# Kernel optimization log

Measured on AMD Instinct MI355X. Metric: run time of the kernel, lower is better.

## Reference

```python
import jax, jax.numpy as jnp
import numpy as np

SCALE = 64 ** 0.5  # hardcoded in original module regardless of dims


def setup_inputs() -> dict:
    key = jax.random.key(0)
    kx, kw = jax.random.split(key)
    B, S, D, O = 8, 2048, 512, 512
    x = jax.random.normal(kx, (B, S, D), dtype=jnp.float32)
    kernel = jax.random.normal(kw, (3, D, O), dtype=jnp.float32) * 0.02
    return {"x": x, "kernel": kernel}


def reference(x, kernel):
    # x: [B, S, D], kernel: [3, D, O]
    WQ = jnp.einsum('bsd,do->bso', x, kernel[0])
    WK = jnp.einsum('bsd,do->bso', x, kernel[1])
    WV = jnp.einsum('bsd,do->bso', x, kernel[2])
    QK = jnp.einsum('bso,bto->bst', WQ, WK)  # [B, S, S]
    # argmin of row-sums, taken from batch element 0 and applied to all batches
    # (faithful to c[0] in the original TF code)
    row_sums = jnp.sum(QK, axis=2)          # [B, S]
    c0 = jnp.argmin(row_sums[0])            # scalar index
    # Original removes row c0, scales, softmaxes remaining rows over last axis,
    # then re-inserts a zero row at c0. Softmax is row-independent, so this is
    # equivalent to softmax on all rows followed by zeroing row c0.
    A = jax.nn.softmax(QK / SCALE, axis=-1)  # [B, S, S]
    row_mask = (jnp.arange(QK.shape[1]) == c0)[None, :, None]
    A = jnp.where(row_mask, jnp.zeros((), A.dtype), A)
    V = jnp.einsum('bst,bto->bso', A, WV)    # [B, S, O]
    return V
```

## Files before the change

kernel.cpp:

```cpp
#include <hip/hip_runtime.h>
#include <stdint.h>

typedef __attribute__((ext_vector_type(8))) short short8;
typedef __attribute__((ext_vector_type(4))) float f32x4;

__device__ __forceinline__ float bf2f(unsigned short u) {
  union { unsigned int i; float f; } x; x.i = ((unsigned int)u) << 16; return x.f;
}
__device__ __forceinline__ unsigned short f2bf(float f) {
  union { float f; unsigned int i; } x; x.f = f;
  unsigned int u = x.i;
  unsigned int r = (u + 0x7FFFu + ((u >> 16) & 1u)) >> 16;
  return (unsigned short)r;
}
__device__ __forceinline__ unsigned int fmono(float f) {
  unsigned int u = __float_as_uint(f);
  return (u & 0x80000000u) ? ~u : (u | 0x80000000u);
}

typedef const __attribute__((address_space(1))) void* gas_ptr;
typedef __attribute__((address_space(3))) void* las_ptr;
__device__ __forceinline__ void gld_lds16(const void* g, void* l) {
  __builtin_amdgcn_global_load_lds((gas_ptr)g, (las_ptr)l, 16, 0, 0);
}

__global__ void cvt_kernel(const float* __restrict__ x, unsigned short* __restrict__ xbf,
                           const float* __restrict__ kern, unsigned short* __restrict__ wbfT) {
  int bid = blockIdx.x;
  if (bid < 4096) {
    int i = bid * 256 + threadIdx.x;
    const float4* xp = (const float4*)x;
    float4 a = xp[2 * i], b = xp[2 * i + 1];
    union { unsigned short us[8]; uint4 v; } o;
    o.us[0] = f2bf(a.x); o.us[1] = f2bf(a.y); o.us[2] = f2bf(a.z); o.us[3] = f2bf(a.w);
    o.us[4] = f2bf(b.x); o.us[5] = f2bf(b.y); o.us[6] = f2bf(b.z); o.us[7] = f2bf(b.w);
    ((uint4*)xbf)[i] = o.v;
  } else {
    __shared__ float tile[32][33];
    int b = bid - 4096;
    int w = b >> 8;
    int r2 = b & 255;
    int d0 = (r2 >> 4) * 32, o0 = (r2 & 15) * 32;
    int c = threadIdx.x & 31, r0 = threadIdx.x >> 5;
    const float* kp = kern + (size_t)w * 262144;
    unsigned short* op = wbfT + (size_t)w * 262144;
#pragma unroll
    for (int i = 0; i < 4; ++i)
      tile[r0 + 8 * i][c] = kp[(size_t)(d0 + r0 + 8 * i) * 512 + o0 + c];
    __syncthreads();
#pragma unroll
    for (int i = 0; i < 4; ++i)
      op[(size_t)(o0 + r0 + 8 * i) * 512 + d0 + c] = f2bf(tile[c][r0 + 8 * i]);
  }
}

template <int MODE, int BNT>
__device__ __forceinline__ void gemm_body(
    int bid, int nwg, char* lds,
    const unsigned short* __restrict__ A, const unsigned short* __restrict__ B,
    void* __restrict__ C, int M, int N, int K,
    long long Abat, long long Bbat, long long Cbat, float scale,
    const unsigned long long* __restrict__ keyp) {
  constexpr int LB = BNT / 128;
  constexpr int BHB = (BNT / 2) * 128;
  constexpr int PBUF = 32768 + 2 * BHB;
  constexpr int WM = (BNT == 128) ? 4 : 2;
  constexpr int RPW = 256 / WM;
  constexpr int MF = RPW / 16;
  constexpr int IC = MF / 4;

  const int tx = N / BNT, ty = M >> 8;
  const int swz = (bid & 7) * (nwg >> 3) + (bid >> 3);
  const int tpz = tx * ty;
  const int z = swz / tpz;
  const int rem = swz - z * tpz;
  const int by = rem / tx;
  const int bx = rem - by * tx;
  const unsigned short* Ab = A + (size_t)z * (size_t)Abat;
  const unsigned short* Bb = B + (size_t)z * (size_t)Bbat;
  const int bm0 = by << 8;
  const int bn0 = bx * BNT;

  const int tid = threadIdx.x, lane = tid & 63, w = tid >> 6;
  const int wr = (WM == 4) ? (w >> 1) : (w >> 2);
  const int wc = (WM == 4) ? (w & 1) : (w & 3);
  const int ln15 = lane & 15, hi = lane >> 4;
  const unsigned xorv = (unsigned)(lane & 7) << 4;
  const unsigned K2 = (unsigned)K * 2;

  const char* gsrc[4];
  gsrc[0] = (const char*)(Ab + (size_t)bm0 * K);
  gsrc[1] = (const char*)(Ab + (size_t)(bm0 + 128) * K);
  gsrc[2] = (const char*)(Bb + (size_t)bn0 * K);
  gsrc[3] = (const char*)(Bb + (size_t)(bn0 + BNT / 2) * K);
  const int hoff_[4] = {0, 16384, 32768, 32768 + BHB};
  unsigned op0 = (unsigned)(w * 1024 + lane * 16);
  unsigned op1 = op0 + 8192;
  const unsigned soff0 = (op0 >> 7) * K2 + ((op0 & 127) ^ (((op0 >> 7) & 7) << 4));
  const unsigned soff1 = (op1 >> 7) * K2 + ((op1 & 127) ^ (((op1 >> 7) & 7) << 4));
  const int lb0 = w * 1024, lb1 = 8192 + w * 1024;

#define STAGE(h, pp, kb)                                              \
  do {                                                                \
    char* lp_ = lds + (pp) * PBUF + hoff_[h];                         \
    const char* gp_ = gsrc[h] + ((unsigned)(kb) << 1);                \
    gld_lds16(gp_ + soff0, lp_ + lb0);                                \
    if ((h) < 2 || LB == 2) gld_lds16(gp_ + soff1, lp_ + lb1);        \
  } while (0)

  f32x4 acc[MF][4];
#pragma unroll
  for (int i = 0; i < MF; ++i)
#pragma unroll
    for (int j = 0; j < 4; ++j) acc[i][j] = (f32x4){0.f, 0.f, 0.f, 0.f};

  f32x4 accs1[MF];
  short8 onesf;
  if constexpr (MODE == 2) {
#pragma unroll
    for (int i = 0; i < MF; ++i) accs1[i] = (f32x4){0.f, 0.f, 0.f, 0.f};
#pragma unroll
    for (int j = 0; j < 8; ++j) onesf[j] = (short)0x3F80;
  }

  const int NT = K >> 6;
  STAGE(0, 0, 0);
  STAGE(1, 0, 0);
  STAGE(2, 0, 0);
  STAGE(3, 0, 0);
  asm volatile("s_waitcnt vmcnt(0)" ::: "memory");
  __builtin_amdgcn_s_barrier();

  short8 bfrag[4][2];
  for (int t = 0; t < NT; ++t) {
    const int p = t & 1;
    char* Lp = lds + p * PBUF;
    const int kN = (t + 1) << 6;
    const bool sN = (t + 1 < NT);
#pragma unroll
    for (int q = 0; q < 4; ++q) {
      if (q == 0) {
#pragma unroll
        for (int nf = 0; nf < 4; ++nf) {
          const int col = wc * 64 + nf * 16 + ln15;
          const char* bp = Lp + 32768 + ((col >= BNT / 2) ? BHB : 0) +
                           (col & (BNT / 2 - 1)) * 128;
#pragma unroll
          for (int k = 0; k < 2; ++k)
            bfrag[nf][k] = *(const short8*)(bp + (((unsigned)(k * 64 + hi * 16)) ^ xorv));
        }
      }
      short8 af[IC][2];
#pragma unroll
      for (int i = 0; i < IC; ++i) {
        const int row = wr * RPW + (q * IC + i) * 16 + ln15;
        const char* ap = Lp + ((row >> 7) << 14) + (row & 127) * 128;
#pragma unroll
        for (int k = 0; k < 2; ++k)
          af[i][k] = *(const short8*)(ap + (((unsigned)(k * 64 + hi * 16)) ^ xorv));
      }
      if (q == 0 && sN) { STAGE(0, p ^ 1, kN); STAGE(2, p ^ 1, kN); }
      if (q == 1 && sN) { STAGE(1, p ^ 1, kN); STAGE(3, p ^ 1, kN); }
      __builtin_amdgcn_s_setprio(1);
#pragma unroll
      for (int i = 0; i < IC; ++i) {
#pragma unroll
        for (int nf = 0; nf < 4; ++nf)
#pragma unroll
          for (int k = 0; k < 2; ++k)
            acc[q * IC + i][nf] = __builtin_amdgcn_mfma_f32_16x16x32_bf16(
                af[i][k], bfrag[nf][k], acc[q * IC + i][nf], 0, 0, 0);
        if constexpr (MODE == 2) {
#pragma unroll
          for (int k = 0; k < 2; ++k)
            accs1[q * IC + i] = __builtin_amdgcn_mfma_f32_16x16x32_bf16(
                af[i][k], onesf, accs1[q * IC + i], 0, 0, 0);
        }
      }
      __builtin_amdgcn_s_setprio(0);
    }
    asm volatile("s_waitcnt vmcnt(0) lgkmcnt(0)" ::: "memory");
    __builtin_amdgcn_s_barrier();
  }
#undef STAGE

  const int rg = hi * 4;
  const int cc = ln15;
  int c0 = 0;
  if constexpr (MODE == 2) c0 = (int)(unsigned int)(*keyp & 0xffffffffULL);
#pragma unroll
  for (int mf = 0; mf < MF; ++mf) {
#pragma unroll
    for (int nf = 0; nf < 4; ++nf) {
#pragma unroll
      for (int r = 0; r < 4; ++r) {
        int m = bm0 + wr * RPW + mf * 16 + rg + r;
        int n = bn0 + wc * 64 + nf * 16 + cc;
        float v = acc[mf][nf][r];
        if (MODE == 0) {
          ((unsigned short*)C)[(size_t)z * (size_t)Cbat + (size_t)m * N + n] =
              f2bf(__expf(v * scale));
        } else if (MODE == 1) {
          int bb = n >> 11, tl = n & 2047;
          ((unsigned short*)C)[((size_t)(bb * 512 + m) << 11) + tl] = f2bf(v);
        } else if (MODE == 2) {
          float lv = (m == c0) ? 0.f : (1.f / accs1[mf][r]);
          ((float*)C)[(size_t)z * (size_t)Cbat + (size_t)m * N + n] = v * lv;
        } else {
          size_t idx = (size_t)(n >> 9) * 8388608 + (size_t)m * 512 + (n & 511);
          float sc = (n >> 9) ? 1.0f : 0.125f;
          ((unsigned short*)C)[idx] = f2bf(v * sc);
        }
      }
    }
  }
}

template <int MODE, int BNT>
__global__ __launch_bounds__(512, 1) void gemm8p(
    const unsigned short* __restrict__ A, const unsigned short* __restrict__ B,
    void* __restrict__ C, int M, int N, int K,
    long long Abat, long long Bbat, long long Cbat, float scale,
    const unsigned long long* __restrict__ keyp) {
  constexpr int PBUF = 32768 + 2 * ((BNT / 2) * 128);
  __shared__ __align__(16) char lds[2 * PBUF];
  gemm_body<MODE, BNT>(blockIdx.x, gridDim.x, lds, A, B, C, M, N, K,
                       Abat, Bbat, Cbat, scale, keyp);
}

__global__ __launch_bounds__(512, 1) void proj_fused(
    const unsigned short* __restrict__ xbf, const unsigned short* __restrict__ wbfT,
    unsigned short* __restrict__ WQ, unsigned short* __restrict__ VT) {
  __shared__ __align__(16) char lds[131072];
  int bid = blockIdx.x;
  if (bid < 256) {
    gemm_body<3, 256>(bid, 256, lds, xbf, wbfT, WQ, 16384, 1024, 512,
                      0, 0, 0, 1.0f, nullptr);
  } else {
    gemm_body<1, 128>(bid - 256, 256, lds, wbfT + 524288, xbf, VT, 512, 16384, 512,
                      0, 0, 0, 1.0f, nullptr);
  }
}

__global__ void ksum_kernel(const unsigned short* __restrict__ WK, float* __restrict__ partial) {
  int col = threadIdx.x;
  int t0 = blockIdx.x * 64;
  float s = 0.f;
  for (int t = 0; t < 64; ++t) s += bf2f(WK[(size_t)(t0 + t) * 512 + col]);
  partial[blockIdx.x * 512 + col] = s;
}

__global__ void rs_argmin_kernel(const unsigned short* __restrict__ WQ,
                                 const float* __restrict__ partial,
                                 unsigned long long* __restrict__ key) {
  __shared__ __align__(16) float ks[512];
  int tid = threadIdx.x;
  for (int c = tid; c < 512; c += 256) {
    float s = 0.f;
#pragma unroll
    for (int j = 0; j < 32; ++j) s += partial[j * 512 + c];
    ks[c] = s;
  }
  __syncthreads();
  int w = tid >> 6, lane = tid & 63;
  float4 ka = *(const float4*)&ks[lane * 8];
  float4 kb = *(const float4*)&ks[lane * 8 + 4];
  for (int it = 0; it < 16; ++it) {
    int row = blockIdx.x * 64 + w * 16 + it;
    uint4 q = *(const uint4*)(WQ + (size_t)row * 512 + lane * 8);
    float d = 0.f;
    d += bf2f((unsigned short)(q.x & 0xffff)) * ka.x;
    d += bf2f((unsigned short)(q.x >> 16)) * ka.y;
    d += bf2f((unsigned short)(q.y & 0xffff)) * ka.z;
    d += bf2f((unsigned short)(q.y >> 16)) * ka.w;
    d += bf2f((unsigned short)(q.z & 0xffff)) * kb.x;
    d += bf2f((unsigned short)(q.z >> 16)) * kb.y;
    d += bf2f((unsigned short)(q.w & 0xffff)) * kb.z;
    d += bf2f((unsigned short)(q.w >> 16)) * kb.w;
#pragma unroll
    for (int m = 32; m; m >>= 1) d += __shfl_xor(d, m);
    if (lane == 0) {
      unsigned long long kk = ((unsigned long long)fmono(d) << 32) | (unsigned int)row;
      atomicMin(key, kk);
    }
  }
}

extern "C" void kernel_launch(void* const* d_in, const int* in_sizes, int n_in,
                              void* d_out, int out_size, void* d_ws, size_t ws_size,
                              hipStream_t stream) {
  const float* x = (const float*)d_in[0];
  const float* kern = (const float*)d_in[1];
  float* out = (float*)d_out;

  char* ws = (char*)d_ws;
  size_t off = 0;
  auto alloc = [&](size_t b) -> char* {
    char* p = ws + off;
    off += (b + 255) & ~(size_t)255;
    return p;
  };
  unsigned short* xbf = (unsigned short*)alloc(16384ull * 512 * 2);
  unsigned short* wbfT = (unsigned short*)alloc(3ull * 512 * 512 * 2);
  unsigned short* WQ = (unsigned short*)alloc(16384ull * 512 * 2);
  unsigned short* WK = (unsigned short*)alloc(16384ull * 512 * 2);
  unsigned short* VT = (unsigned short*)alloc(16384ull * 512 * 2);
  float* partial = (float*)alloc(32ull * 512 * 4);
  unsigned long long* key = (unsigned long long*)alloc(256);
  size_t fixed = off;
  size_t sbytes = 2048ull * 2048 * 2;
  int nb = 1;
  if (ws_size > fixed + sbytes) {
    size_t av = (ws_size - fixed) / sbytes;
    nb = av > 8 ? 8 : (int)av;
    if (nb < 1) nb = 1;
  }
  unsigned short* S = (unsigned short*)alloc(sbytes * (size_t)nb);

  hipMemsetAsync(key, 0xFF, 8, stream);

  cvt_kernel<<<4864, 256, 0, stream>>>(x, xbf, kern, wbfT);

  proj_fused<<<512, 512, 0, stream>>>(xbf, wbfT, WQ, VT);

  ksum_kernel<<<32, 512, 0, stream>>>(WK, partial);
  rs_argmin_kernel<<<32, 256, 0, stream>>>(WQ, partial, key);

  for (int b0 = 0; b0 < 8; b0 += nb) {
    int cb = (8 - b0) < nb ? (8 - b0) : nb;
    gemm8p<0, 256><<<64 * cb, 512, 0, stream>>>(
        WQ + (size_t)b0 * 2048 * 512, WK + (size_t)b0 * 2048 * 512, S,
        2048, 2048, 512, 2048ll * 512, 2048ll * 512, 2048ll * 2048, 1.0f,
        nullptr);
    gemm8p<2, 128><<<32 * cb, 512, 0, stream>>>(
        S, VT + (size_t)b0 * 512 * 2048, out + (size_t)b0 * 2048 * 512,
        2048, 512, 2048, 2048ll * 2048, 512ll * 2048, 2048ll * 512, 1.0f,
        key);
  }
}
```

Baseline: 162.2 us.

## Split K across wave pairs in PV GEMM with LDS reduction

Replaces the generic MODE 2 path of the shared GEMM body with a dedicated P·V kernel. In it, wave pairs split each 64-wide K step, each wave taking half the K slice, instead of every wave computing its full row set over all of K. Partial accumulators and row-sum accumulators are exchanged through LDS, summed, and each wave then writes half of the output rows with normalization and row-c0 zeroing. The goal is fewer serial MFMA and LDS fragment reads per wave and a smaller per-wave accumulator footprint. The cost is an extra LDS reduction phase with barriers at the end.

```diff
diff --git a/kernel.cpp b/kernel.cpp
--- a/kernel.cpp
+++ b/kernel.cpp
@@ -114,15 +114,6 @@
 #pragma unroll
     for (int j = 0; j < 4; ++j) acc[i][j] = (f32x4){0.f, 0.f, 0.f, 0.f};
 
-  f32x4 accs1[MF];
-  short8 onesf;
-  if constexpr (MODE == 2) {
-#pragma unroll
-    for (int i = 0; i < MF; ++i) accs1[i] = (f32x4){0.f, 0.f, 0.f, 0.f};
-#pragma unroll
-    for (int j = 0; j < 8; ++j) onesf[j] = (short)0x3F80;
-  }
-
   const int NT = K >> 6;
   STAGE(0, 0, 0);
   STAGE(1, 0, 0);
@@ -170,12 +161,6 @@
           for (int k = 0; k < 2; ++k)
             acc[q * IC + i][nf] = __builtin_amdgcn_mfma_f32_16x16x32_bf16(
                 af[i][k], bfrag[nf][k], acc[q * IC + i][nf], 0, 0, 0);
-        if constexpr (MODE == 2) {
-#pragma unroll
-          for (int k = 0; k < 2; ++k)
-            accs1[q * IC + i] = __builtin_amdgcn_mfma_f32_16x16x32_bf16(
-                af[i][k], onesf, accs1[q * IC + i], 0, 0, 0);
-        }
       }
       __builtin_amdgcn_s_setprio(0);
     }
@@ -186,8 +171,6 @@
 
   const int rg = hi * 4;
   const int cc = ln15;
-  int c0 = 0;
-  if constexpr (MODE == 2) c0 = (int)(unsigned int)(*keyp & 0xffffffffULL);
 #pragma unroll
   for (int mf = 0; mf < MF; ++mf) {
 #pragma unroll
@@ -203,9 +186,6 @@
         } else if (MODE == 1) {
           int bb = n >> 11, tl = n & 2047;
           ((unsigned short*)C)[((size_t)(bb * 512 + m) << 11) + tl] = f2bf(v);
-        } else if (MODE == 2) {
-          float lv = (m == c0) ? 0.f : (1.f / accs1[mf][r]);
-          ((float*)C)[(size_t)z * (size_t)Cbat + (size_t)m * N + n] = v * lv;
         } else {
           size_t idx = (size_t)(n >> 9) * 8388608 + (size_t)m * 512 + (n & 511);
           float sc = (n >> 9) ? 1.0f : 0.125f;
@@ -239,6 +219,165 @@
   } else {
     gemm_body<1, 128>(bid - 256, 256, lds, wbfT + 524288, xbf, VT, 512, 16384, 512,
                       0, 0, 0, 1.0f, nullptr);
+  }
+}
+
+__global__ __launch_bounds__(512, 1) void gemm_pv(
+    const unsigned short* __restrict__ A, const unsigned short* __restrict__ B,
+    float* __restrict__ C, int N, long long Abat, long long Bbat, long long Cbat,
+    const unsigned long long* __restrict__ keyp) {
+  constexpr int PBUF = 49152;
+  __shared__ __align__(16) char lds[2 * PBUF];
+  const int K = 2048;
+  const int tx = N >> 7;
+  const int nwg = gridDim.x;
+  const int bid = blockIdx.x;
+  const int swz = (bid & 7) * (nwg >> 3) + (bid >> 3);
+  const int tpz = tx * 8;
+  const int z = swz / tpz;
+  const int rem = swz - z * tpz;
+  const int by = rem / tx;
+  const int bx = rem - by * tx;
+  const unsigned short* Ab = A + (size_t)z * (size_t)Abat;
+  const unsigned short* Bb = B + (size_t)z * (size_t)Bbat;
+  const int bm0 = by << 8;
+  const int bn0 = bx << 7;
+
+  const int tid = threadIdx.x, lane = tid & 63, w = tid >> 6;
+  const int wk = w & 1, wc = (w >> 1) & 1, wr = w >> 2;
+  const int ln15 = lane & 15, hi = lane >> 4;
+  const unsigned xorv = (unsigned)(lane & 7) << 4;
+  const unsigned K2 = (unsigned)K * 2;
+
+  const char* gsrc[4];
+  gsrc[0] = (const char*)(Ab + (size_t)bm0 * K);
+  gsrc[1] = (const char*)(Ab + (size_t)(bm0 + 128) * K);
+  gsrc[2] = (const char*)(Bb + (size_t)bn0 * K);
+  gsrc[3] = (const char*)(Bb + (size_t)(bn0 + 64) * K);
+  const int hoff_[4] = {0, 16384, 32768, 40960};
+  unsigned op0 = (unsigned)(w * 1024 + lane * 16);
+  unsigned op1 = op0 + 8192;
+  const unsigned soff0 = (op0 >> 7) * K2 + ((op0 & 127) ^ (((op0 >> 7) & 7) << 4));
+  const unsigned soff1 = (op1 >> 7) * K2 + ((op1 & 127) ^ (((op1 >> 7) & 7) << 4));
+  const int lb0 = w * 1024, lb1 = 8192 + w * 1024;
+
+#define STAGE(h, pp, kb)                                              \
+  do {                                                                \
+    char* lp_ = lds + (pp) * PBUF + hoff_[h];                         \
+    const char* gp_ = gsrc[h] + ((unsigned)(kb) << 1);                \
+    gld_lds16(gp_ + soff0, lp_ + lb0);                                \
+    if ((h) < 2) gld_lds16(gp_ + soff1, lp_ + lb1);                   \
+  } while (0)
+
+  f32x4 acc[8][4];
+  f32x4 accs1[8];
+#pragma unroll
+  for (int i = 0; i < 8; ++i) {
+#pragma unroll
+    for (int j = 0; j < 4; ++j) acc[i][j] = (f32x4){0.f, 0.f, 0.f, 0.f};
+    accs1[i] = (f32x4){0.f, 0.f, 0.f, 0.f};
+  }
+  short8 onesf;
+#pragma unroll
+  for (int j = 0; j < 8; ++j) onesf[j] = (short)0x3F80;
+
+  const unsigned koff = ((unsigned)(wk * 64 + hi * 16)) ^ xorv;
+
+  const int NT = 32;
+  STAGE(0, 0, 0);
+  STAGE(1, 0, 0);
+  STAGE(2, 0, 0);
+  STAGE(3, 0, 0);
+  asm volatile("s_waitcnt vmcnt(0)" ::: "memory");
+  __builtin_amdgcn_s_barrier();
+
+  short8 bfrag[4];
+  for (int t = 0; t < NT; ++t) {
+    const int p = t & 1;
+    char* Lp = lds + p * PBUF;
+    const int kN = (t + 1) << 6;
+    const bool sN = (t + 1 < NT);
+#pragma unroll
+    for (int q = 0; q < 4; ++q) {
+      if (q == 0) {
+#pragma unroll
+        for (int nf = 0; nf < 4; ++nf) {
+          const int col = wc * 64 + nf * 16 + ln15;
+          const char* bp = Lp + 32768 + ((col >= 64) ? 8192 : 0) + (col & 63) * 128;
+          bfrag[nf] = *(const short8*)(bp + koff);
+        }
+      }
+      short8 af[2];
+#pragma unroll
+      for (int i = 0; i < 2; ++i) {
+        const int row = wr * 128 + (q * 2 + i) * 16 + ln15;
+        const char* ap = Lp + ((row >> 7) << 14) + (row & 127) * 128;
+        af[i] = *(const short8*)(ap + koff);
+      }
+      if (q == 0 && sN) { STAGE(0, p ^ 1, kN); STAGE(2, p ^ 1, kN); }
+      if (q == 1 && sN) { STAGE(1, p ^ 1, kN); STAGE(3, p ^ 1, kN); }
+      __builtin_amdgcn_s_setprio(1);
+#pragma unroll
+      for (int i = 0; i < 2; ++i) {
+#pragma unroll
+        for (int nf = 0; nf < 4; ++nf)
+          acc[q * 2 + i][nf] = __builtin_amdgcn_mfma_f32_16x16x32_bf16(
+              af[i], bfrag[nf], acc[q * 2 + i][nf], 0, 0, 0);
+        accs1[q * 2 + i] = __builtin_amdgcn_mfma_f32_16x16x32_bf16(
+            af[i], onesf, accs1[q * 2 + i], 0, 0, 0);
+      }
+      __builtin_amdgcn_s_setprio(0);
+    }
+    asm volatile("s_waitcnt vmcnt(0) lgkmcnt(0)" ::: "memory");
+    __builtin_amdgcn_s_barrier();
+  }
+#undef STAGE
+
+  const int give0 = wk ? 0 : 4;
+  const int recv0 = wk ? 4 : 0;
+  char* wp = lds + w * 12288 + lane * 192;
+  const char* rp = lds + (w ^ 1) * 12288 + lane * 192;
+#pragma unroll
+  for (int r2 = 0; r2 < 2; ++r2) {
+#pragma unroll
+    for (int m2 = 0; m2 < 2; ++m2) {
+#pragma unroll
+      for (int nf = 0; nf < 4; ++nf)
+        *(f32x4*)(wp + (m2 * 4 + nf) * 16) = acc[give0 + r2 * 2 + m2][nf];
+      *(f32x4*)(wp + (8 + m2) * 16) = accs1[give0 + r2 * 2 + m2];
+    }
+    asm volatile("s_waitcnt lgkmcnt(0)" ::: "memory");
+    __builtin_amdgcn_s_barrier();
+#pragma unroll
+    for (int m2 = 0; m2 < 2; ++m2) {
+#pragma unroll
+      for (int nf = 0; nf < 4; ++nf) {
+        f32x4 pv = *(const f32x4*)(rp + (m2 * 4 + nf) * 16);
+        acc[recv0 + r2 * 2 + m2][nf] += pv;
+      }
+      f32x4 ps = *(const f32x4*)(rp + (8 + m2) * 16);
+      accs1[recv0 + r2 * 2 + m2] += ps;
+    }
+    asm volatile("s_waitcnt lgkmcnt(0)" ::: "memory");
+    __builtin_amdgcn_s_barrier();
+  }
+
+  const int rg = hi * 4;
+  const int cc = ln15;
+  const int c0 = (int)(unsigned int)(*keyp & 0xffffffffULL);
+#pragma unroll
+  for (int kf = 0; kf < 4; ++kf) {
+    const int mf = recv0 + kf;
+#pragma unroll
+    for (int nf = 0; nf < 4; ++nf) {
+#pragma unroll
+      for (int r = 0; r < 4; ++r) {
+        int m = bm0 + wr * 128 + mf * 16 + rg + r;
+        int n = bn0 + wc * 64 + nf * 16 + cc;
+        float lv = (m == c0) ? 0.f : (1.f / accs1[mf][r]);
+        C[(size_t)z * (size_t)Cbat + (size_t)m * N + n] = acc[mf][nf][r] * lv;
+      }
+    }
   }
 }
 
@@ -332,9 +471,9 @@
         WQ + (size_t)b0 * 2048 * 512, WK + (size_t)b0 * 2048 * 512, S,
         2048, 2048, 512, 2048ll * 512, 2048ll * 512, 2048ll * 2048, 1.0f,
         nullptr);
-    gemm8p<2, 128><<<32 * cb, 512, 0, stream>>>(
+    gemm_pv<<<32 * cb, 512, 0, stream>>>(
         S, VT + (size_t)b0 * 512 * 2048, out + (size_t)b0 * 2048 * 512,
-        2048, 512, 2048, 2048ll * 2048, 512ll * 2048, 2048ll * 512, 1.0f,
+        512, 2048ll * 2048, 512ll * 2048, 2048ll * 512,
         key);
   }
 }
```

New measurement: 226.9 us. 39.8% more time.

## Store exp scores and V in fp8 and run PV GEMM with fp8 MFMA

Applied to the files above, without the earlier changes.

The exponentiated score matrix is now written as fp8 (e4m3) instead of bf16, halving its memory traffic. V is stored as a two-term fp8 split (high part plus residual), and a new dedicated fp8 PV GEMM kernel uses the fp8 MFMA instruction with row sums computed via a ones vector. This cuts S write/read bandwidth and uses faster fp8 matrix instructions, at the cost of reduced precision for the softmax probabilities and extra MFMAs for the V residual.

```diff
diff --git a/kernel.cpp b/kernel.cpp
--- a/kernel.cpp
+++ b/kernel.cpp
@@ -3,6 +3,7 @@
 
 typedef __attribute__((ext_vector_type(8))) short short8;
 typedef __attribute__((ext_vector_type(4))) float f32x4;
+typedef long long i64;
 
 __device__ __forceinline__ float bf2f(unsigned short u) {
   union { unsigned int i; float f; } x; x.i = ((unsigned int)u) << 16; return x.f;
@@ -16,6 +17,28 @@
 __device__ __forceinline__ unsigned int fmono(float f) {
   unsigned int u = __float_as_uint(f);
   return (u & 0x80000000u) ? ~u : (u | 0x80000000u);
+}
+
+__device__ __forceinline__ unsigned char f2fp8(float f) {
+  unsigned int u = __float_as_uint(f);
+  unsigned int s = (u >> 24) & 0x80u;
+  unsigned int av = u & 0x7fffffffu;
+  if (av >= 0x43E00000u) return (unsigned char)(s | 0x7E);
+  if (av < 0x3C800000u) {
+    int mi = (int)rintf(fabsf(__uint_as_float(av)) * 512.f);
+    return (unsigned char)(s | (unsigned)mi);
+  }
+  unsigned int r = av + 0x7FFFFu + ((av >> 20) & 1u);
+  unsigned int e = (r >> 23) - 120u;
+  unsigned int m3 = (r >> 20) & 7u;
+  if (e > 15u) return (unsigned char)(s | 0x7E);
+  return (unsigned char)(s | (e << 3) | m3);
+}
+__device__ __forceinline__ float fp8dec(unsigned char b) {
+  int s = b >> 7, e = (b >> 3) & 15, m = b & 7;
+  float v = e ? __uint_as_float(((unsigned)(e + 120) << 23) | ((unsigned)m << 20))
+              : (float)m * 0.001953125f;
+  return s ? -v : v;
 }
 
 typedef const __attribute__((address_space(1))) void* gas_ptr;
@@ -59,8 +82,7 @@
     int bid, int nwg, char* lds,
     const unsigned short* __restrict__ A, const unsigned short* __restrict__ B,
     void* __restrict__ C, int M, int N, int K,
-    long long Abat, long long Bbat, long long Cbat, float scale,
-    const unsigned long long* __restrict__ keyp) {
+    long long Abat, long long Bbat, long long Cbat, float scale) {
   constexpr int LB = BNT / 128;
   constexpr int BHB = (BNT / 2) * 128;
   constexpr int PBUF = 32768 + 2 * BHB;
@@ -114,15 +136,6 @@
 #pragma unroll
     for (int j = 0; j < 4; ++j) acc[i][j] = (f32x4){0.f, 0.f, 0.f, 0.f};
 
-  f32x4 accs1[MF];
-  short8 onesf;
-  if constexpr (MODE == 2) {
-#pragma unroll
-    for (int i = 0; i < MF; ++i) accs1[i] = (f32x4){0.f, 0.f, 0.f, 0.f};
-#pragma unroll
-    for (int j = 0; j < 8; ++j) onesf[j] = (short)0x3F80;
-  }
-
   const int NT = K >> 6;
   STAGE(0, 0, 0);
   STAGE(1, 0, 0);
@@ -170,12 +183,6 @@
           for (int k = 0; k < 2; ++k)
             acc[q * IC + i][nf] = __builtin_amdgcn_mfma_f32_16x16x32_bf16(
                 af[i][k], bfrag[nf][k], acc[q * IC + i][nf], 0, 0, 0);
-        if constexpr (MODE == 2) {
-#pragma unroll
-          for (int k = 0; k < 2; ++k)
-            accs1[q * IC + i] = __builtin_amdgcn_mfma_f32_16x16x32_bf16(
-                af[i][k], onesf, accs1[q * IC + i], 0, 0, 0);
-        }
       }
       __builtin_amdgcn_s_setprio(0);
     }
@@ -186,8 +193,6 @@
 
   const int rg = hi * 4;
   const int cc = ln15;
-  int c0 = 0;
-  if constexpr (MODE == 2) c0 = (int)(unsigned int)(*keyp & 0xffffffffULL);
 #pragma unroll
   for (int mf = 0; mf < MF; ++mf) {
 #pragma unroll
@@ -198,14 +203,14 @@
         int n = bn0 + wc * 64 + nf * 16 + cc;
         float v = acc[mf][nf][r];
         if (MODE == 0) {
-          ((unsigned short*)C)[(size_t)z * (size_t)Cbat + (size_t)m * N + n] =
-              f2bf(__expf(v * scale));
+          ((unsigned char*)C)[(size_t)z * (size_t)Cbat + (size_t)m * N + n] =
+              f2fp8(__expf(v * scale));
         } else if (MODE == 1) {
           int bb = n >> 11, tl = n & 2047;
-          ((unsigned short*)C)[((size_t)(bb * 512 + m) << 11) + tl] = f2bf(v);
-        } else if (MODE == 2) {
-          float lv = (m == c0) ? 0.f : (1.f / accs1[mf][r]);
-          ((float*)C)[(size_t)z * (size_t)Cbat + (size_t)m * N + n] = v * lv;
+          size_t idx = ((size_t)(bb * 512 + m) << 11) + tl;
+          unsigned char bhi = f2fp8(v);
+          ((unsigned char*)C)[idx] = bhi;
+          ((unsigned char*)C)[idx + 8388608] = f2fp8(v - fp8dec(bhi));
         } else {
           size_t idx = (size_t)(n >> 9) * 8388608 + (size_t)m * 512 + (n & 511);
           float sc = (n >> 9) ? 1.0f : 0.125f;
@@ -220,25 +225,153 @@
 __global__ __launch_bounds__(512, 1) void gemm8p(
     const unsigned short* __restrict__ A, const unsigned short* __restrict__ B,
     void* __restrict__ C, int M, int N, int K,
-    long long Abat, long long Bbat, long long Cbat, float scale,
-    const unsigned long long* __restrict__ keyp) {
+    long long Abat, long long Bbat, long long Cbat, float scale) {
   constexpr int PBUF = 32768 + 2 * ((BNT / 2) * 128);
   __shared__ __align__(16) char lds[2 * PBUF];
   gemm_body<MODE, BNT>(blockIdx.x, gridDim.x, lds, A, B, C, M, N, K,
-                       Abat, Bbat, Cbat, scale, keyp);
+                       Abat, Bbat, Cbat, scale);
 }
 
 __global__ __launch_bounds__(512, 1) void proj_fused(
     const unsigned short* __restrict__ xbf, const unsigned short* __restrict__ wbfT,
-    unsigned short* __restrict__ WQ, unsigned short* __restrict__ VT) {
+    unsigned short* __restrict__ WQ, unsigned char* __restrict__ VT) {
   __shared__ __align__(16) char lds[131072];
   int bid = blockIdx.x;
   if (bid < 256) {
     gemm_body<3, 256>(bid, 256, lds, xbf, wbfT, WQ, 16384, 1024, 512,
-                      0, 0, 0, 1.0f, nullptr);
+                      0, 0, 0, 1.0f);
   } else {
     gemm_body<1, 128>(bid - 256, 256, lds, wbfT + 524288, xbf, VT, 512, 16384, 512,
-                      0, 0, 0, 1.0f, nullptr);
+                      0, 0, 0, 1.0f);
+  }
+}
+
+__global__ __launch_bounds__(512, 1) void gemm_pv8(
+    const unsigned char* __restrict__ S8, const unsigned char* __restrict__ V8,
+    float* __restrict__ C, const unsigned long long* __restrict__ keyp) {
+  constexpr int PBUF = 65536;
+  __shared__ __align__(16) char lds[2 * PBUF];
+  const int nwg = gridDim.x;
+  const int bid = blockIdx.x;
+  const int swz = (bid & 7) * (nwg >> 3) + (bid >> 3);
+  const int z = swz >> 5;
+  const int rem = swz & 31;
+  const int by = rem >> 2;
+  const int bx = rem & 3;
+  const unsigned char* Ab = S8 + (size_t)z * 4194304;
+  const unsigned char* Bh = V8 + (size_t)z * 1048576;
+  const int bm0 = by << 8;
+  const int bn0 = bx << 7;
+
+  const int tid = threadIdx.x, lane = tid & 63, w = tid >> 6;
+  const int wr = w >> 1, wc = w & 1;
+  const int ln15 = lane & 15, hi = lane >> 4;
+  const unsigned xorv = (unsigned)(lane & 7) << 4;
+
+  const unsigned char* gsrc[6];
+  gsrc[0] = Ab + (size_t)bm0 * 2048;
+  gsrc[1] = Ab + (size_t)(bm0 + 128) * 2048;
+  gsrc[2] = Bh + (size_t)bn0 * 2048;
+  gsrc[3] = Bh + (size_t)(bn0 + 64) * 2048;
+  gsrc[4] = gsrc[2] + 8388608;
+  gsrc[5] = gsrc[3] + 8388608;
+  const int hoff_[6] = {0, 16384, 32768, 40960, 49152, 57344};
+  unsigned op0 = (unsigned)(w * 1024 + lane * 16);
+  unsigned op1 = op0 + 8192;
+  const unsigned soff0 = (op0 >> 7) * 2048 + ((op0 & 127) ^ (((op0 >> 7) & 7) << 4));
+  const unsigned soff1 = (op1 >> 7) * 2048 + ((op1 & 127) ^ (((op1 >> 7) & 7) << 4));
+  const int lb0 = w * 1024, lb1 = 8192 + w * 1024;
+
+#define STAGE8(h, pp, kb)                                             \
+  do {                                                                \
+    char* lp_ = lds + (pp) * PBUF + hoff_[h];                         \
+    const unsigned char* gp_ = gsrc[h] + (unsigned)(kb);              \
+    gld_lds16(gp_ + soff0, lp_ + lb0);                                \
+    if ((h) < 2) gld_lds16(gp_ + soff1, lp_ + lb1);                   \
+  } while (0)
+
+  f32x4 acc[4][4];
+  f32x4 accs1[4];
+#pragma unroll
+  for (int i = 0; i < 4; ++i) {
+#pragma unroll
+    for (int j = 0; j < 4; ++j) acc[i][j] = (f32x4){0.f, 0.f, 0.f, 0.f};
+    accs1[i] = (f32x4){0.f, 0.f, 0.f, 0.f};
+  }
+  const i64 ones8 = 0x3838383838383838LL;
+
+  const int NT = 16;
+  STAGE8(0, 0, 0); STAGE8(1, 0, 0); STAGE8(2, 0, 0);
+  STAGE8(3, 0, 0); STAGE8(4, 0, 0); STAGE8(5, 0, 0);
+  asm volatile("s_waitcnt vmcnt(0)" ::: "memory");
+  __builtin_amdgcn_s_barrier();
+
+  i64 bh[4][4], bl[4][4];
+  for (int t = 0; t < NT; ++t) {
+    const int p = t & 1;
+    char* Lp = lds + p * PBUF;
+    const int kN = (t + 1) << 7;
+    const bool sN = (t + 1 < NT);
+#pragma unroll
+    for (int q = 0; q < 4; ++q) {
+      if (q == 0) {
+#pragma unroll
+        for (int nf = 0; nf < 4; ++nf) {
+          const int col = wc * 64 + nf * 16 + ln15;
+          const char* bp = Lp + 32768 + ((col >= 64) ? 8192 : 0) + (col & 63) * 128;
+#pragma unroll
+          for (int ks = 0; ks < 4; ++ks) {
+            const unsigned off = ((unsigned)(ks * 32 + hi * 8)) ^ xorv;
+            bh[nf][ks] = *(const i64*)(bp + off);
+            bl[nf][ks] = *(const i64*)(bp + 16384 + off);
+          }
+        }
+      }
+      i64 af[4];
+      {
+        const int row = wr * 64 + q * 16 + ln15;
+        const char* ap = Lp + ((row >> 7) << 14) + (row & 127) * 128;
+#pragma unroll
+        for (int ks = 0; ks < 4; ++ks)
+          af[ks] = *(const i64*)(ap + ((((unsigned)(ks * 32 + hi * 8)) ^ xorv)));
+      }
+      if (q == 0 && sN) { STAGE8(0, p ^ 1, kN); STAGE8(2, p ^ 1, kN); STAGE8(4, p ^ 1, kN); }
+      if (q == 1 && sN) { STAGE8(1, p ^ 1, kN); STAGE8(3, p ^ 1, kN); STAGE8(5, p ^ 1, kN); }
+      __builtin_amdgcn_s_setprio(1);
+#pragma unroll
+      for (int ks = 0; ks < 4; ++ks) {
+#pragma unroll
+        for (int nf = 0; nf < 4; ++nf) {
+          acc[q][nf] = __builtin_amdgcn_mfma_f32_16x16x32_fp8_fp8(
+              af[ks], bh[nf][ks], acc[q][nf], 0, 0, 0);
+          acc[q][nf] = __builtin_amdgcn_mfma_f32_16x16x32_fp8_fp8(
+              af[ks], bl[nf][ks], acc[q][nf], 0, 0, 0);
+        }
+        accs1[q] = __builtin_amdgcn_mfma_f32_16x16x32_fp8_fp8(
+            af[ks], ones8, accs1[q], 0, 0, 0);
+      }
+      __builtin_amdgcn_s_setprio(0);
+    }
+    asm volatile("s_waitcnt vmcnt(0) lgkmcnt(0)" ::: "memory");
+    __builtin_amdgcn_s_barrier();
+  }
+#undef STAGE8
+
+  const int rg = hi * 4;
+  const int cc = ln15;
+  const int c0 = (int)(unsigned int)(*keyp & 0xffffffffULL);
+#pragma unroll
+  for (int mf = 0; mf < 4; ++mf) {
+#pragma unroll
+    for (int nf = 0; nf < 4; ++nf) {
+#pragma unroll
+      for (int r = 0; r < 4; ++r) {
+        int m = bm0 + wr * 64 + mf * 16 + rg + r;
+        int n = bn0 + wc * 64 + nf * 16 + cc;
+        float lv = (m == c0) ? 0.f : (1.f / accs1[mf][r]);
+        C[(size_t)z * 1048576 + (size_t)m * 512 + n] = acc[mf][nf][r] * lv;
+      }
+    }
   }
 }
 
@@ -304,18 +437,18 @@
   unsigned short* wbfT = (unsigned short*)alloc(3ull * 512 * 512 * 2);
   unsigned short* WQ = (unsigned short*)alloc(16384ull * 512 * 2);
   unsigned short* WK = (unsigned short*)alloc(16384ull * 512 * 2);
-  unsigned short* VT = (unsigned short*)alloc(16384ull * 512 * 2);
+  unsigned char* VT = (unsigned char*)alloc(2ull * 8388608);
   float* partial = (float*)alloc(32ull * 512 * 4);
   unsigned long long* key = (unsigned long long*)alloc(256);
   size_t fixed = off;
-  size_t sbytes = 2048ull * 2048 * 2;
+  size_t sbytes = 2048ull * 2048;
   int nb = 1;
   if (ws_size > fixed + sbytes) {
     size_t av = (ws_size - fixed) / sbytes;
     nb = av > 8 ? 8 : (int)av;
     if (nb < 1) nb = 1;
   }
-  unsigned short* S = (unsigned short*)alloc(sbytes * (size_t)nb);
+  unsigned char* S = (unsigned char*)alloc(sbytes * (size_t)nb);
 
   hipMemsetAsync(key, 0xFF, 8, stream);
 
@@ -330,11 +463,8 @@
     int cb = (8 - b0) < nb ? (8 - b0) : nb;
     gemm8p<0, 256><<<64 * cb, 512, 0, stream>>>(
         WQ + (size_t)b0 * 2048 * 512, WK + (size_t)b0 * 2048 * 512, S,
-        2048, 2048, 512, 2048ll * 512, 2048ll * 512, 2048ll * 2048, 1.0f,
-        nullptr);
-    gemm8p<2, 128><<<32 * cb, 512, 0, stream>>>(
-        S, VT + (size_t)b0 * 512 * 2048, out + (size_t)b0 * 2048 * 512,
-        2048, 512, 2048, 2048ll * 2048, 512ll * 2048, 2048ll * 512, 1.0f,
-        key);
-  }
-}
+        2048, 2048, 512, 2048ll * 512, 2048ll * 512, 2048ll * 2048, 1.0f);
+    gemm_pv8<<<32 * cb, 512, 0, stream>>>(
+        S, VT + (size_t)b0 * 1048576, out + (size_t)b0 * 2048 * 512, key);
+  }
+}
```

After: 206.5 us. +27.3%, slower.
